# Kernel optimization log

Hardware: AMD Instinct MI355X
Metric: run time of the kernel (lower is better)

Reference implementation:

```python
import jax, jax.numpy as jnp
import numpy as np

VOCAB = 32000
EMB = 32
HID = 16
SEQ = 128
BATCH = 32


def setup_inputs() -> dict:
    key = jax.random.key(0)
    ks = jax.random.split(key, 7)
    stdv = 1.0 / np.sqrt(HID)
    u = lambda k, shape: jax.random.uniform(k, shape, jnp.float32, -stdv, stdv)
    return {
        "input_batch": jax.random.randint(ks[0], (SEQ, BATCH), 0, VOCAB),
        "h0": jax.random.normal(ks[1], (BATCH, HID), jnp.float32),
        "embedding": u(ks[2], (VOCAB, EMB)),
        "W_ih": u(ks[3], (HID, EMB + HID)),
        "b_ih": u(ks[4], (HID,)),
        "W_ho": u(ks[5], (VOCAB, HID)),
        "b_ho": u(ks[6], (VOCAB,)),
    }


def reference(input_batch, h0, embedding, W_ih, b_ih, W_ho, b_ho):
    # Embedding lookup for all timesteps: [S, B, EMB]
    emb_seq = embedding[input_batch]

    def step(h, x_t):
        # Torch code detaches both input and hidden before the cell (.data)
        combined = jax.lax.stop_gradient(jnp.concatenate([x_t, h], axis=1))  # [B, EMB+HID]
        h_new = jnp.tanh(combined @ W_ih.T + b_ih)                           # [B, HID]
        logits = h_new @ W_ho.T + b_ho                                       # [B, VOCAB]
        out = jax.nn.log_softmax(logits, axis=-1)
        return h_new, out

    _, predictions = jax.lax.scan(step, h0, emb_seq)  # [S, B, VOCAB]
    return predictions
```

## Files before the change

kernel.cpp:

```cpp
#include <hip/hip_runtime.h>
#include <math.h>

#define VOCAB 32000
#define EMB   32
#define HID   16
#define SEQ   128
#define BATCH 32
#define ROWS  (SEQ*BATCH)
#define WIH_LD (EMB+HID)
#define VBLK  2048
#define NVB   16
#define KPT   8
#define RCH   128
#define NRC   32

__global__ __launch_bounds__(256) void k_embed(const int* __restrict__ tok,
    const float* __restrict__ emb, const float* __restrict__ Wih,
    const float* __restrict__ bih, float* __restrict__ X)
{
    __shared__ float sW[HID][EMB];
    __shared__ float sb[HID];
    int t = threadIdx.x;
    for (int i = t; i < HID*EMB; i += 256)
        sW[i/EMB][i%EMB] = Wih[(i/EMB)*WIH_LD + (i%EMB)];
    if (t < HID) sb[t] = bih[t];
    __syncthreads();

    int row = blockIdx.x*256 + t;
    int token = tok[row];
    float x[EMB];
    const float4* ep = (const float4*)(emb + (long)token*EMB);
    #pragma unroll
    for (int q = 0; q < EMB/4; ++q) {
        float4 v = ep[q];
        x[4*q+0]=v.x; x[4*q+1]=v.y; x[4*q+2]=v.z; x[4*q+3]=v.w;
    }
    #pragma unroll
    for (int j = 0; j < HID; ++j) {
        float acc = sb[j];
        #pragma unroll
        for (int e = 0; e < EMB; ++e) acc = fmaf(sW[j][e], x[e], acc);
        X[row*HID + j] = acc;
    }
}

__global__ __launch_bounds__(512) void k_rnn(const float* __restrict__ X,
    const float* __restrict__ h0, const float* __restrict__ Wih,
    float* __restrict__ H)
{
    __shared__ float sWh[HID][HID];
    __shared__ float h[BATCH][HID];
    int t = threadIdx.x;
    if (t < HID*HID)
        sWh[t/HID][t%HID] = Wih[(t/HID)*WIH_LD + EMB + (t%HID)];
    h[t>>4][t&15] = h0[t];
    __syncthreads();

    int b = t >> 4, j = t & 15;
    for (int s = 0; s < SEQ; ++s) {
        int row = s*BATCH + b;
        float acc = X[row*HID + j];
        #pragma unroll
        for (int k = 0; k < HID; ++k) acc = fmaf(sWh[j][k], h[b][k], acc);
        float e2 = __expf(fminf(2.f*acc, 30.f));
        float hn = (e2 - 1.f) / (e2 + 1.f);
        __syncthreads();
        h[b][j] = hn;
        H[row*HID + j] = hn;
        __syncthreads();
    }
}

__global__ __launch_bounds__(256, 2) void k_sumexp(const float* __restrict__ Who,
    const float* __restrict__ bho, const float* __restrict__ H,
    float* __restrict__ part)
{
    int t = threadIdx.x;
    int vblk = blockIdx.x;
    float w[KPT][HID]; float bb[KPT];
    #pragma unroll
    for (int k = 0; k < KPT; ++k) {
        int v = vblk*VBLK + t + 256*k;
        if (v < VOCAB) {
            const float4* wp = (const float4*)(Who + (long)v*HID);
            #pragma unroll
            for (int q = 0; q < 4; ++q) {
                float4 f = wp[q];
                w[k][4*q+0]=f.x; w[k][4*q+1]=f.y; w[k][4*q+2]=f.z; w[k][4*q+3]=f.w;
            }
            bb[k] = bho[v];
        } else {
            #pragma unroll
            for (int i = 0; i < HID; ++i) w[k][i] = 0.f;
            bb[k] = -1e30f;
        }
    }

    for (int r = 0; r < RCH; ++r) {
        int row = blockIdx.y*RCH + r;
        float h[HID];
        const float4* hp = (const float4*)(H + row*HID);
        #pragma unroll
        for (int q = 0; q < 4; ++q) {
            float4 f = hp[q];
            h[4*q+0]=f.x; h[4*q+1]=f.y; h[4*q+2]=f.z; h[4*q+3]=f.w;
        }
        float p = 0.f;
        #pragma unroll
        for (int k = 0; k < KPT; ++k) {
            float acc = bb[k];
            #pragma unroll
            for (int i = 0; i < HID; ++i) acc = fmaf(w[k][i], h[i], acc);
            p += __expf(acc);
        }
        #pragma unroll
        for (int off = 32; off > 0; off >>= 1) p += __shfl_xor(p, off, 64);
        if ((t & 63) == 0)
            part[row*64 + vblk*4 + (t>>6)] = p;
    }
}

__global__ __launch_bounds__(256) void k_logl(const float* __restrict__ part,
    float* __restrict__ logl)
{
    int t = threadIdx.x;
    int row = blockIdx.x*4 + (t>>6);
    int lane = t & 63;
    float p = part[row*64 + lane];
    #pragma unroll
    for (int off = 32; off > 0; off >>= 1) p += __shfl_xor(p, off, 64);
    if (lane == 0) logl[row] = logf(p);
}

__global__ __launch_bounds__(256, 2) void k_write(const float* __restrict__ Who,
    const float* __restrict__ bho, const float* __restrict__ H,
    const float* __restrict__ logl, float* __restrict__ out)
{
    int t = threadIdx.x;
    int vblk = blockIdx.x;
    float w[KPT][HID]; float bb[KPT]; int vv[KPT];
    #pragma unroll
    for (int k = 0; k < KPT; ++k) {
        int v = vblk*VBLK + t + 256*k; vv[k] = v;
        if (v < VOCAB) {
            const float4* wp = (const float4*)(Who + (long)v*HID);
            #pragma unroll
            for (int q = 0; q < 4; ++q) {
                float4 f = wp[q];
                w[k][4*q+0]=f.x; w[k][4*q+1]=f.y; w[k][4*q+2]=f.z; w[k][4*q+3]=f.w;
            }
            bb[k] = bho[v];
        } else {
            #pragma unroll
            for (int i = 0; i < HID; ++i) w[k][i] = 0.f;
            bb[k] = 0.f;
        }
    }

    for (int r = 0; r < RCH; ++r) {
        int row = blockIdx.y*RCH + r;
        float h[HID];
        const float4* hp = (const float4*)(H + row*HID);
        #pragma unroll
        for (int q = 0; q < 4; ++q) {
            float4 f = hp[q];
            h[4*q+0]=f.x; h[4*q+1]=f.y; h[4*q+2]=f.z; h[4*q+3]=f.w;
        }
        float ll = logl[row];
        float* orow = out + (long)row*VOCAB;
        #pragma unroll
        for (int k = 0; k < KPT; ++k) {
            if (vv[k] < VOCAB) {
                float acc = bb[k];
                #pragma unroll
                for (int i = 0; i < HID; ++i) acc = fmaf(w[k][i], h[i], acc);
                orow[vv[k]] = acc - ll;
            }
        }
    }
}

extern "C" void kernel_launch(void* const* d_in, const int* in_sizes, int n_in,
                              void* d_out, int out_size, void* d_ws, size_t ws_size,
                              hipStream_t stream)
{
    const int*   tok = (const int*)  d_in[0];
    const float* h0  = (const float*)d_in[1];
    const float* emb = (const float*)d_in[2];
    const float* Wih = (const float*)d_in[3];
    const float* bih = (const float*)d_in[4];
    const float* Who = (const float*)d_in[5];
    const float* bho = (const float*)d_in[6];
    float* out = (float*)d_out;

    char* ws = (char*)d_ws;
    float* X    = (float*)(ws);
    float* H    = (float*)(ws + 262144);
    float* part = (float*)(ws + 524288);
    float* logl = (float*)(ws + 1572864);

    k_embed <<<dim3(ROWS/256), 256, 0, stream>>>(tok, emb, Wih, bih, X);
    k_rnn   <<<dim3(1), 512, 0, stream>>>(X, h0, Wih, H);
    k_sumexp<<<dim3(NVB, NRC), 256, 0, stream>>>(Who, bho, H, part);
    k_logl  <<<dim3(ROWS/4), 256, 0, stream>>>(part, logl);
    k_write <<<dim3(NVB, NRC), 256, 0, stream>>>(Who, bho, H, logl, out);
}
```

Measured before the change: 742.0 us.

## Vectorize logit writes, double-buffer RNN state, pair rows in sum-exp pass

The output-writing kernel now gives each thread four consecutive vocab entries and stores them as one float4, replacing scattered scalar stores. This targets the 524 MB output write, which dominates runtime. The RNN kernel double-buffers the hidden state to drop one barrier per step and prefetches the next timestep's input. The sum-exp kernel processes two rows per iteration to reuse loaded weights, and the embed kernel uses 128-thread blocks; both the sum-exp and write kernels keep 128 weight floats per thread in registers, which may raise register pressure.

```diff
diff --git a/kernel.cpp b/kernel.cpp
--- a/kernel.cpp
+++ b/kernel.cpp
@@ -10,23 +10,22 @@
 #define WIH_LD (EMB+HID)
 #define VBLK  2048
 #define NVB   16
-#define KPT   8
 #define RCH   128
 #define NRC   32
 
-__global__ __launch_bounds__(256) void k_embed(const int* __restrict__ tok,
+__global__ __launch_bounds__(128) void k_embed(const int* __restrict__ tok,
     const float* __restrict__ emb, const float* __restrict__ Wih,
     const float* __restrict__ bih, float* __restrict__ X)
 {
     __shared__ float sW[HID][EMB];
     __shared__ float sb[HID];
     int t = threadIdx.x;
-    for (int i = t; i < HID*EMB; i += 256)
+    for (int i = t; i < HID*EMB; i += 128)
         sW[i/EMB][i%EMB] = Wih[(i/EMB)*WIH_LD + (i%EMB)];
     if (t < HID) sb[t] = bih[t];
     __syncthreads();
 
-    int row = blockIdx.x*256 + t;
+    int row = blockIdx.x*128 + t;
     int token = tok[row];
     float x[EMB];
     const float4* ep = (const float4*)(emb + (long)token*EMB);
@@ -49,25 +48,27 @@
     float* __restrict__ H)
 {
     __shared__ float sWh[HID][HID];
-    __shared__ float h[BATCH][HID];
+    __shared__ float h[2][BATCH][HID];
     int t = threadIdx.x;
     if (t < HID*HID)
         sWh[t/HID][t%HID] = Wih[(t/HID)*WIH_LD + EMB + (t%HID)];
-    h[t>>4][t&15] = h0[t];
+    h[0][t>>4][t&15] = h0[t];
     __syncthreads();
 
     int b = t >> 4, j = t & 15;
+    int cur = 0;
+    float x = X[t];
     for (int s = 0; s < SEQ; ++s) {
-        int row = s*BATCH + b;
-        float acc = X[row*HID + j];
-        #pragma unroll
-        for (int k = 0; k < HID; ++k) acc = fmaf(sWh[j][k], h[b][k], acc);
+        float xn = (s+1 < SEQ) ? X[(s+1)*512 + t] : 0.f;
+        float acc = x;
+        #pragma unroll
+        for (int k = 0; k < HID; ++k) acc = fmaf(sWh[j][k], h[cur][b][k], acc);
         float e2 = __expf(fminf(2.f*acc, 30.f));
         float hn = (e2 - 1.f) / (e2 + 1.f);
+        h[cur^1][b][j] = hn;
+        H[s*512 + t] = hn;
         __syncthreads();
-        h[b][j] = hn;
-        H[row*HID + j] = hn;
-        __syncthreads();
+        x = xn; cur ^= 1;
     }
 }
 
@@ -77,22 +78,107 @@
 {
     int t = threadIdx.x;
     int vblk = blockIdx.x;
-    float w[KPT][HID]; float bb[KPT];
-    #pragma unroll
-    for (int k = 0; k < KPT; ++k) {
-        int v = vblk*VBLK + t + 256*k;
-        if (v < VOCAB) {
-            const float4* wp = (const float4*)(Who + (long)v*HID);
+    float w[2][4][HID]; float bb[2][4];
+    #pragma unroll
+    for (int g = 0; g < 2; ++g) {
+        int base = vblk*VBLK + g*1024 + 4*t;
+        #pragma unroll
+        for (int c = 0; c < 4; ++c) {
+            int v = base + c;
+            if (v < VOCAB) {
+                const float4* wp = (const float4*)(Who + (long)v*HID);
+                #pragma unroll
+                for (int q = 0; q < 4; ++q) {
+                    float4 f = wp[q];
+                    w[g][c][4*q+0]=f.x; w[g][c][4*q+1]=f.y;
+                    w[g][c][4*q+2]=f.z; w[g][c][4*q+3]=f.w;
+                }
+                bb[g][c] = bho[v];
+            } else {
+                #pragma unroll
+                for (int i = 0; i < HID; ++i) w[g][c][i] = 0.f;
+                bb[g][c] = -1e30f;
+            }
+        }
+    }
+
+    int wid = t >> 6, lane = t & 63;
+    for (int r = 0; r < RCH; r += 2) {
+        int row0 = blockIdx.y*RCH + r;
+        float h0[HID], h1[HID];
+        const float4* hp0 = (const float4*)(H + row0*HID);
+        const float4* hp1 = (const float4*)(H + (row0+1)*HID);
+        #pragma unroll
+        for (int q = 0; q < 4; ++q) {
+            float4 f0 = hp0[q], f1 = hp1[q];
+            h0[4*q+0]=f0.x; h0[4*q+1]=f0.y; h0[4*q+2]=f0.z; h0[4*q+3]=f0.w;
+            h1[4*q+0]=f1.x; h1[4*q+1]=f1.y; h1[4*q+2]=f1.z; h1[4*q+3]=f1.w;
+        }
+        float p0 = 0.f, p1 = 0.f;
+        #pragma unroll
+        for (int g = 0; g < 2; ++g)
+        #pragma unroll
+        for (int c = 0; c < 4; ++c) {
+            float a0 = bb[g][c], a1 = bb[g][c];
             #pragma unroll
-            for (int q = 0; q < 4; ++q) {
-                float4 f = wp[q];
-                w[k][4*q+0]=f.x; w[k][4*q+1]=f.y; w[k][4*q+2]=f.z; w[k][4*q+3]=f.w;
-            }
-            bb[k] = bho[v];
-        } else {
-            #pragma unroll
-            for (int i = 0; i < HID; ++i) w[k][i] = 0.f;
-            bb[k] = -1e30f;
+            for (int i = 0; i < HID; ++i) {
+                a0 = fmaf(w[g][c][i], h0[i], a0);
+                a1 = fmaf(w[g][c][i], h1[i], a1);
+            }
+            p0 += __expf(a0);
+            p1 += __expf(a1);
+        }
+        #pragma unroll
+        for (int off = 32; off > 0; off >>= 1) {
+            p0 += __shfl_xor(p0, off, 64);
+            p1 += __shfl_xor(p1, off, 64);
+        }
+        if (lane == 0) {
+            part[(long)row0*64     + vblk*4 + wid] = p0;
+            part[(long)(row0+1)*64 + vblk*4 + wid] = p1;
+        }
+    }
+}
+
+__global__ __launch_bounds__(256) void k_logl(const float* __restrict__ part,
+    float* __restrict__ logl)
+{
+    int t = threadIdx.x;
+    int row = blockIdx.x*4 + (t>>6);
+    int lane = t & 63;
+    float p = part[row*64 + lane];
+    #pragma unroll
+    for (int off = 32; off > 0; off >>= 1) p += __shfl_xor(p, off, 64);
+    if (lane == 0) logl[row] = logf(p);
+}
+
+__global__ __launch_bounds__(256, 2) void k_write(const float* __restrict__ Who,
+    const float* __restrict__ bho, const float* __restrict__ H,
+    const float* __restrict__ logl, float* __restrict__ out)
+{
+    int t = threadIdx.x;
+    int vblk = blockIdx.x;
+    float w[2][4][HID]; float bb[2][4];
+    #pragma unroll
+    for (int g = 0; g < 2; ++g) {
+        int base = vblk*VBLK + g*1024 + 4*t;
+        #pragma unroll
+        for (int c = 0; c < 4; ++c) {
+            int v = base + c;
+            if (v < VOCAB) {
+                const float4* wp = (const float4*)(Who + (long)v*HID);
+                #pragma unroll
+                for (int q = 0; q < 4; ++q) {
+                    float4 f = wp[q];
+                    w[g][c][4*q+0]=f.x; w[g][c][4*q+1]=f.y;
+                    w[g][c][4*q+2]=f.z; w[g][c][4*q+3]=f.w;
+                }
+                bb[g][c] = bho[v];
+            } else {
+                #pragma unroll
+                for (int i = 0; i < HID; ++i) w[g][c][i] = 0.f;
+                bb[g][c] = 0.f;
+            }
         }
     }
 
@@ -105,76 +191,22 @@
             float4 f = hp[q];
             h[4*q+0]=f.x; h[4*q+1]=f.y; h[4*q+2]=f.z; h[4*q+3]=f.w;
         }
-        float p = 0.f;
-        #pragma unroll
-        for (int k = 0; k < KPT; ++k) {
-            float acc = bb[k];
-            #pragma unroll
-            for (int i = 0; i < HID; ++i) acc = fmaf(w[k][i], h[i], acc);
-            p += __expf(acc);
-        }
-        #pragma unroll
-        for (int off = 32; off > 0; off >>= 1) p += __shfl_xor(p, off, 64);
-        if ((t & 63) == 0)
-            part[row*64 + vblk*4 + (t>>6)] = p;
-    }
-}
-
-__global__ __launch_bounds__(256) void k_logl(const float* __restrict__ part,
-    float* __restrict__ logl)
-{
-    int t = threadIdx.x;
-    int row = blockIdx.x*4 + (t>>6);
-    int lane = t & 63;
-    float p = part[row*64 + lane];
-    #pragma unroll
-    for (int off = 32; off > 0; off >>= 1) p += __shfl_xor(p, off, 64);
-    if (lane == 0) logl[row] = logf(p);
-}
-
-__global__ __launch_bounds__(256, 2) void k_write(const float* __restrict__ Who,
-    const float* __restrict__ bho, const float* __restrict__ H,
-    const float* __restrict__ logl, float* __restrict__ out)
-{
-    int t = threadIdx.x;
-    int vblk = blockIdx.x;
-    float w[KPT][HID]; float bb[KPT]; int vv[KPT];
-    #pragma unroll
-    for (int k = 0; k < KPT; ++k) {
-        int v = vblk*VBLK + t + 256*k; vv[k] = v;
-        if (v < VOCAB) {
-            const float4* wp = (const float4*)(Who + (long)v*HID);
-            #pragma unroll
-            for (int q = 0; q < 4; ++q) {
-                float4 f = wp[q];
-                w[k][4*q+0]=f.x; w[k][4*q+1]=f.y; w[k][4*q+2]=f.z; w[k][4*q+3]=f.w;
-            }
-            bb[k] = bho[v];
-        } else {
-            #pragma unroll
-            for (int i = 0; i < HID; ++i) w[k][i] = 0.f;
-            bb[k] = 0.f;
-        }
-    }
-
-    for (int r = 0; r < RCH; ++r) {
-        int row = blockIdx.y*RCH + r;
-        float h[HID];
-        const float4* hp = (const float4*)(H + row*HID);
-        #pragma unroll
-        for (int q = 0; q < 4; ++q) {
-            float4 f = hp[q];
-            h[4*q+0]=f.x; h[4*q+1]=f.y; h[4*q+2]=f.z; h[4*q+3]=f.w;
-        }
         float ll = logl[row];
         float* orow = out + (long)row*VOCAB;
         #pragma unroll
-        for (int k = 0; k < KPT; ++k) {
-            if (vv[k] < VOCAB) {
-                float acc = bb[k];
-                #pragma unroll
-                for (int i = 0; i < HID; ++i) acc = fmaf(w[k][i], h[i], acc);
-                orow[vv[k]] = acc - ll;
+        for (int g = 0; g < 2; ++g) {
+            int base = vblk*VBLK + g*1024 + 4*t;
+            float acc[4];
+            #pragma unroll
+            for (int c = 0; c < 4; ++c) {
+                float a = bb[g][c];
+                #pragma unroll
+                for (int i = 0; i < HID; ++i) a = fmaf(w[g][c][i], h[i], a);
+                acc[c] = a - ll;
+            }
+            if (base < VOCAB) {
+                float4 o; o.x=acc[0]; o.y=acc[1]; o.z=acc[2]; o.w=acc[3];
+                *(float4*)(orow + base) = o;
             }
         }
     }
@@ -199,7 +231,7 @@
     float* part = (float*)(ws + 524288);
     float* logl = (float*)(ws + 1572864);
 
-    k_embed <<<dim3(ROWS/256), 256, 0, stream>>>(tok, emb, Wih, bih, X);
+    k_embed <<<dim3(ROWS/128), 128, 0, stream>>>(tok, emb, Wih, bih, X);
     k_rnn   <<<dim3(1), 512, 0, stream>>>(X, h0, Wih, H);
     k_sumexp<<<dim3(NVB, NRC), 256, 0, stream>>>(Who, bho, H, part);
     k_logl  <<<dim3(ROWS/4), 256, 0, stream>>>(part, logl);
```

Result: faster. 713.0 us (-3.9%).
